# Kernel optimization log

Measured on AMD Instinct MI355X. Metric: run time of the kernel, lower is better.

The kernel has to match this reference:

```python
import jax, jax.numpy as jnp
import numpy as np

L, B, D = 2048, 16, 1024
SCALE_X = (1.0 + 2.0 * float(np.exp(0.0))) ** 0.5  # rescale=True, highway_bias=0 -> sqrt(3)


def setup_inputs() -> dict:
    key = jax.random.key(0)
    k1, k2, k3 = jax.random.split(key, 3)
    x = jax.random.normal(k1, (L, B, D), dtype=jnp.float32)
    c0 = jnp.zeros((B, D), dtype=jnp.float32)
    # Xavier-ish scale (3/d)^0.5 as in reset_parameters
    val_range = (3.0 / D) ** 0.5
    weight = jax.random.uniform(k2, (D, 3 * D), dtype=jnp.float32,
                                minval=-val_range, maxval=val_range)
    weight_c = jax.random.uniform(k3, (2 * D,), dtype=jnp.float32,
                                  minval=-val_range, maxval=val_range)
    bias = jnp.zeros((2 * D,), dtype=jnp.float32)
    return {"x": x, "c0": c0, "weight": weight, "weight_c": weight_c, "bias": bias}


def _sru_forward(x, c0, weight, weight_c, bias):
    # u = x @ W, viewed as [L, B, D, 3] (k = 3)
    u = jnp.einsum('lbi,io->lbo', x, weight).reshape(L, B, D, 3)
    fw, rw = weight_c[:D], weight_c[D:]      # per-feature recurrent gate weights
    fb, rb = bias[:D], bias[D:]              # forget / reset biases
    u0 = u[..., 0]                           # [L, B, D] candidate
    u1 = u[..., 1] + fb                      # forget pre-activation
    u2 = u[..., 2] + rb                      # reset pre-activation
    xp = x * SCALE_X                         # highway term (k==3, skip via x)

    def step(c_prev, inputs):
        u0_t, u1_t, u2_t, xp_t = inputs
        f = jax.nn.sigmoid(u1_t + c_prev * fw)
        r = jax.nn.sigmoid(u2_t + c_prev * rw)
        c = u0_t + (c_prev - u0_t) * f
        g = c  # activation_type == 0 (identity)
        h = xp_t + (g - xp_t) * r
        return c, h

    c_final, h = jax.lax.scan(step, c0, (u0, u1, u2, xp))
    return h, c_final


def reference(x, c0, weight, weight_c, bias):
    return _sru_forward(x, c0, weight, weight_c, bias)
```

## Files before the change

kernel.cpp:

```cpp
#include <hip/hip_runtime.h>
#include <stdint.h>

#define L_DIM 2048
#define B_DIM 16
#define D_DIM 1024
#define M_DIM 32768
#define K_DIM 1024
#define N_DIM 3072
#define SCALE_X 1.7320508075688772f

typedef __attribute__((ext_vector_type(8))) short short8;
typedef __attribute__((ext_vector_type(8))) unsigned short ushort8;
typedef __attribute__((ext_vector_type(4))) float f32x4;

__device__ __forceinline__ float bf2f(uint32_t b) {
    union { uint32_t u; float f; } v; v.u = b << 16; return v.f;
}
__device__ __forceinline__ uint16_t f2bf(float f) {
    union { float f; uint32_t u; } v; v.f = f;
    uint32_t u = v.u;
    return (uint16_t)((u + 0x7FFFu + ((u >> 16) & 1u)) >> 16);
}

__device__ __forceinline__ void gl16(const uint16_t* g, uint16_t* l) {
    __builtin_amdgcn_global_load_lds(
        (const __attribute__((address_space(1))) void*)g,
        (__attribute__((address_space(3))) void*)l,
        16 , 0, 0);
}

__device__ __forceinline__ void fence_all() {
    asm volatile("" ::: "memory");
    __builtin_amdgcn_sched_barrier(0);
}
__device__ __forceinline__ void barrier_hard() {
    fence_all();
    __builtin_amdgcn_s_barrier();
    fence_all();
}

__global__ void __launch_bounds__(256)
prep_w_kernel(const float* __restrict__ w, uint16_t* __restrict__ wt) {
    __shared__ uint16_t tile[32][33];
    int bid = blockIdx.x;
    int kt = (bid & 31) * 32;
    int nt = (bid >> 5) * 32;
    int tx = threadIdx.x & 31;
    int ty = threadIdx.x >> 5;
#pragma unroll
    for (int r = 0; r < 32; r += 8)
        tile[ty + r][tx] = f2bf(w[(size_t)(kt + ty + r) * N_DIM + nt + tx]);
    __syncthreads();
#pragma unroll
    for (int r = 0; r < 32; r += 8)
        wt[(size_t)(nt + ty + r) * K_DIM + kt + tx] = tile[tx][ty + r];
}

__global__ void __launch_bounds__(256)
prep_x_kernel(const float* __restrict__ x, uint16_t* __restrict__ xb) {
    size_t i = (size_t)blockIdx.x * 256 + threadIdx.x;
    const float4 a = *(const float4*)(x + i * 8);
    const float4 b = *(const float4*)(x + i * 8 + 4);
    ushort8 o;
    o[0] = f2bf(a.x); o[1] = f2bf(a.y); o[2] = f2bf(a.z); o[3] = f2bf(a.w);
    o[4] = f2bf(b.x); o[5] = f2bf(b.y); o[6] = f2bf(b.z); o[7] = f2bf(b.w);
    *(ushort8*)(xb + i * 8) = o;
}

__global__ void __launch_bounds__(512, 2)
gemm_8ph_kernel(const uint16_t* __restrict__ Ab,
                const uint16_t* __restrict__ Bt,
                uint16_t* __restrict__ u01,
                uint16_t* __restrict__ u2p)
{
    __shared__ uint16_t lds[65536];

    int bid = blockIdx.x;
    int mg = bid / 96;
    int tt = bid - mg * 96;
    int ntile = tt >> 3;
    int mtile = mg * 8 + (tt & 7);
    int m0 = mtile * 256;
    int n0 = ntile * 256;

    int t = threadIdx.x;
    int lane = t & 63;
    int w = t >> 6;
    int wm = (w >> 2) * 128;
    int wn = (w & 3) * 64;

    int row0 = t >> 3;
    int slot = t & 7;
    int swz_c = (slot ^ (row0 & 7)) * 8;
    const uint16_t* pA = Ab + (((size_t)(m0 + row0)) << 10) + swz_c;
    const uint16_t* pB = Bt + (((size_t)(n0 + row0)) << 10) + swz_c;

    int frow = lane & 15;
    int fkb = (lane >> 4) * 16;

    f32x4 acc[8][4] = {};
    short8 aF[4][2];
    short8 bF[4][2];

#define STAGE(hh, Tn) { \
    const uint16_t* gs = (((hh) < 2) ? pA : pB) + ((size_t)((hh) & 1) * 131072) + (size_t)(Tn) * 64; \
    uint16_t* ld = lds + nxtO + (hh) * 8192 + t * 8; \
    gl16(gs, ld); gl16(gs + 65536, ld + 4096); }

#define RD_A(mh) { \
    _Pragma("unroll") for (int mf = 0; mf < 4; mf++) \
    _Pragma("unroll") for (int ks = 0; ks < 2; ks++) { \
        int r = wm + (mh) * 64 + mf * 16 + frow; \
        int cb = (ks * 64 + fkb) ^ ((r & 7) << 4); \
        aF[mf][ks] = *(const short8*)(lds + curA + r * 64 + (cb >> 1)); } }

#define RD_B() { \
    _Pragma("unroll") for (int nf = 0; nf < 4; nf++) \
    _Pragma("unroll") for (int ks = 0; ks < 2; ks++) { \
        int r = wn + nf * 16 + frow; \
        int cb = (ks * 64 + fkb) ^ ((r & 7) << 4); \
        bF[nf][ks] = *(const short8*)(lds + curB + r * 64 + (cb >> 1)); } }

#define QM(mh, nh) { \
    __builtin_amdgcn_s_setprio(1); \
    _Pragma("unroll") for (int mf = 0; mf < 4; mf++) \
    _Pragma("unroll") for (int nj = 0; nj < 2; nj++) \
    _Pragma("unroll") for (int ks = 0; ks < 2; ks++) \
        acc[(mh) * 4 + mf][(nh) * 2 + nj] = __builtin_amdgcn_mfma_f32_16x16x32_bf16( \
            aF[mf][ks], bF[(nh) * 2 + nj][ks], acc[(mh) * 4 + mf][(nh) * 2 + nj], 0, 0, 0); \
    __builtin_amdgcn_s_setprio(0); }

    {
        int nxtO = 0;
        STAGE(0, 0); STAGE(1, 0); STAGE(2, 0); STAGE(3, 0);
    }

    for (int T = 0; T < 15; ++T) {
        int cur = T & 1;
        int curA = cur * 32768;
        int curB = curA + 16384;
        int nxtO = (cur ^ 1) * 32768;

        barrier_hard();
        STAGE(0, T + 1);
        fence_all();
        asm volatile("s_waitcnt vmcnt(2)" ::: "memory");
        barrier_hard();
        RD_B();
        RD_A(0);
        QM(0, 0);
        fence_all();
        STAGE(1, T + 1);
        fence_all();
        QM(0, 1);
        RD_A(1);
        fence_all();
        STAGE(2, T + 1);
        fence_all();
        QM(1, 1);
        fence_all();
        STAGE(3, T + 1);
        fence_all();
        QM(1, 0);
    }

    {
        int curA = 32768;
        int curB = curA + 16384;
        barrier_hard();
        asm volatile("s_waitcnt vmcnt(0)" ::: "memory");
        barrier_hard();
        RD_B();
        RD_A(0);
        QM(0, 0);
        QM(0, 1);
        RD_A(1);
        QM(1, 1);
        QM(1, 0);
    }

#undef STAGE
#undef RD_A
#undef RD_B
#undef QM

    int colf = lane & 15;
    int rowq = (lane >> 4) * 4;
#pragma unroll
    for (int i = 0; i < 8; i++) {
#pragma unroll
        for (int j = 0; j < 4; j++) {
            int gcol = n0 + wn + j * 16 + colf;
            int dq = gcol / 3;
            int cm = gcol - dq * 3;
#pragma unroll
            for (int r = 0; r < 4; r++) {
                int grow = m0 + wm + i * 16 + rowq + r;
                uint16_t v = f2bf(acc[i][j][r]);
                if (cm < 2) u01[(size_t)grow * 2048 + dq * 2 + cm] = v;
                else        u2p[(size_t)grow * 1024 + dq] = v;
            }
        }
    }
}

__global__ void __launch_bounds__(256)
gemm_kernel(const float* __restrict__ A32,
            const uint16_t* __restrict__ Bt,
            uint16_t* __restrict__ u01,
            uint16_t* __restrict__ u2p)
{
    __shared__ uint16_t As[128 * 32];
    __shared__ uint16_t Bs[128 * 32];

    int bid = blockIdx.x;
    int mg = bid / 192;
    int tt = bid - mg * 192;
    int ntile = tt >> 3;
    int mtile = mg * 8 + (tt & 7);
    int m0 = mtile * 128;
    int n0 = ntile * 128;

    int t = threadIdx.x;
    int lane = t & 63;
    int w = t >> 6;
    int wm = (w >> 1) * 64;
    int wn = (w & 1) * 64;

    f32x4 acc[4][4] = {};

    int frow = lane & 15;
    int fk = (lane >> 4) * 8;

    for (int kt = 0; kt < K_DIM; kt += 32) {
#pragma unroll
        for (int c = 0; c < 4; c++) {
            int idx = c * 256 + t;
            int row = idx >> 3;
            int ko = (idx & 7) * 4;
            float4 v = *(const float4*)(A32 + (size_t)(m0 + row) * K_DIM + kt + ko);
            ushort4 o;
            o.x = f2bf(v.x); o.y = f2bf(v.y); o.z = f2bf(v.z); o.w = f2bf(v.w);
            *(ushort4*)(As + row * 32 + ko) = o;
        }
#pragma unroll
        for (int c = 0; c < 2; c++) {
            int idx = c * 256 + t;
            int row = idx >> 2;
            int ko = (idx & 3) * 8;
            short8 v = *(const short8*)(Bt + (size_t)(n0 + row) * K_DIM + kt + ko);
            *(short8*)(Bs + row * 32 + ko) = v;
        }
        __syncthreads();

        short8 af[4], bfr[4];
#pragma unroll
        for (int i = 0; i < 4; i++) {
            af[i]  = *(const short8*)(As + (wm + i * 16 + frow) * 32 + fk);
            bfr[i] = *(const short8*)(Bs + (wn + i * 16 + frow) * 32 + fk);
        }
#pragma unroll
        for (int i = 0; i < 4; i++)
#pragma unroll
            for (int j = 0; j < 4; j++)
                acc[i][j] = __builtin_amdgcn_mfma_f32_16x16x32_bf16(af[i], bfr[j], acc[i][j], 0, 0, 0);
        __syncthreads();
    }

    int colf = lane & 15;
    int rowq = (lane >> 4) * 4;
#pragma unroll
    for (int i = 0; i < 4; i++) {
#pragma unroll
        for (int j = 0; j < 4; j++) {
            int gcol = n0 + wn + j * 16 + colf;
            int dq = gcol / 3;
            int cm = gcol - dq * 3;
#pragma unroll
            for (int r = 0; r < 4; r++) {
                int grow = m0 + wm + i * 16 + rowq + r;
                uint16_t v = f2bf(acc[i][j][r]);
                if (cm < 2) u01[(size_t)grow * 2048 + dq * 2 + cm] = v;
                else        u2p[(size_t)grow * 1024 + dq] = v;
            }
        }
    }
}

__global__ void __launch_bounds__(64)
scan_c_kernel(const uint32_t* u01,
              uint16_t* u2io,
              const float* __restrict__ c0,
              const float* __restrict__ wc,
              const float* __restrict__ bias,
              float* out)
{
    int cid = blockIdx.x * 64 + threadIdx.x;
    int d = cid & (D_DIM - 1);
    float fw = wc[d], rw = wc[D_DIM + d];
    float fb = bias[d], rb = bias[D_DIM + d];
    float c = c0[cid];

    constexpr int P = 16;
    const int STEP = B_DIM * D_DIM;
    uint32_t b01[P];
    uint16_t b2[P];
#pragma unroll
    for (int j = 0; j < P; j++) {
        b01[j] = u01[cid + j * STEP];
        b2[j]  = u2io[cid + j * STEP];
    }

    for (int lb = 0; lb < L_DIM; lb += P) {
#pragma unroll
        for (int j = 0; j < P; j++) {
            int l = lb + j;
            uint32_t v01 = b01[j];
            float u2 = bf2f((uint32_t)b2[j]);

            int ln = l + P; if (ln > L_DIM - 1) ln = L_DIM - 1;
            b01[j] = u01[cid + ln * STEP];
            b2[j]  = u2io[cid + ln * STEP];

            float u0 = bf2f(v01 & 0xFFFFu);
            float u1 = bf2f(v01 >> 16);
            float cp = c;
            float ef = __expf(-(u1 + fb + cp * fw));
            float f = __builtin_amdgcn_rcpf(1.0f + ef);
            c = u0 + (cp - u0) * f;
            float rarg = u2 + rb + cp * rw;
            out[l * STEP + cid] = c;
            u2io[l * STEP + cid] = f2bf(rarg);
        }
    }
    out[L_DIM * STEP + cid] = c;
}

__global__ void __launch_bounds__(256)
h_kernel(float* out,
         const uint16_t* __restrict__ rargp,
         const float* __restrict__ x)
{
    size_t i = ((size_t)blockIdx.x * 256 + threadIdx.x) * 4;

    f32x4 cv = *(const f32x4*)(out + i);
    f32x4 xv = *(const f32x4*)(x + i);
    ushort4 uv = *(const ushort4*)(rargp + i);

    float ra[4] = { bf2f(uv.x), bf2f(uv.y), bf2f(uv.z), bf2f(uv.w) };
    f32x4 h;
#pragma unroll
    for (int e = 0; e < 4; e++) {
        float xp = xv[e] * SCALE_X;
        float er = __expf(-ra[e]);
        float r = __builtin_amdgcn_rcpf(1.0f + er);
        h[e] = xp + (cv[e] - xp) * r;
    }
    *(f32x4*)(out + i) = h;
}

extern "C" void kernel_launch(void* const* d_in, const int* in_sizes, int n_in,
                              void* d_out, int out_size, void* d_ws, size_t ws_size,
                              hipStream_t stream) {
    const float* x    = (const float*)d_in[0];
    const float* c0   = (const float*)d_in[1];
    const float* w    = (const float*)d_in[2];
    const float* wc   = (const float*)d_in[3];
    const float* bias = (const float*)d_in[4];

    uint16_t* wt  = (uint16_t*)d_ws;
    uint16_t* u2p = (uint16_t*)((char*)d_ws + 6291456);
    const size_t XB_OFF = 6291456 + (size_t)M_DIM * D_DIM * 2;
    const size_t WS_NEED = XB_OFF + (size_t)M_DIM * K_DIM * 2;

    uint16_t* u01 = (uint16_t*)d_out;
    float* out = (float*)d_out;

    prep_w_kernel<<<(K_DIM / 32) * (N_DIM / 32), 256, 0, stream>>>(w, wt);

    if (ws_size >= WS_NEED) {
        uint16_t* xb = (uint16_t*)((char*)d_ws + XB_OFF);
        prep_x_kernel<<<(M_DIM * K_DIM / 8) / 256, 256, 0, stream>>>(x, xb);
        gemm_8ph_kernel<<<(M_DIM / 256) * (N_DIM / 256), 512, 0, stream>>>(xb, wt, u01, u2p);
    } else {
        gemm_kernel<<<(M_DIM / 128) * (N_DIM / 128), 256, 0, stream>>>(x, wt, u01, u2p);
    }

    scan_c_kernel<<<(B_DIM * D_DIM) / 64, 64, 0, stream>>>((const uint32_t*)u01, u2p,
                                                           c0, wc, bias, out);
    h_kernel<<<(M_DIM * D_DIM / 4) / 256, 256, 0, stream>>>(out, u2p, x);
}
```

Measured before the change: 699.4 us.

## Move reset-gate math out of the serial scan and pre-permute weight columns

The weight transpose now permutes output columns so the GEMM epilogue writes u0/u1 interleaved and u2 contiguously, with no per-element divide by 3. The scan no longer reads u2 or computes the reset argument. It only writes packed bf16 (c_prev, c) pairs, which cuts traffic in the latency-bound serial loop. The h kernel recomputes the reset gate from u2, c_prev, rw and rb, and processes 8 elements per thread. The trade-off is lower precision, since c is stored as bf16 before h is formed, and the scan writes into the same output buffer that h_kernel later overwrites.

```diff
diff --git a/kernel.cpp b/kernel.cpp
--- a/kernel.cpp
+++ b/kernel.cpp
@@ -12,6 +12,7 @@
 typedef __attribute__((ext_vector_type(8))) short short8;
 typedef __attribute__((ext_vector_type(8))) unsigned short ushort8;
 typedef __attribute__((ext_vector_type(4))) float f32x4;
+typedef __attribute__((ext_vector_type(4))) unsigned int u32x4;
 
 __device__ __forceinline__ float bf2f(uint32_t b) {
     union { uint32_t u; float f; } v; v.u = b << 16; return v.f;
@@ -37,6 +38,12 @@
     fence_all();
     __builtin_amdgcn_s_barrier();
     fence_all();
+}
+
+__device__ __forceinline__ int perm_n(int n) {
+    int dq = n / 3;
+    int cm = n - dq * 3;
+    return (cm < 2) ? (dq * 2 + cm) : (2048 + dq);
 }
 
 __global__ void __launch_bounds__(256)
@@ -52,8 +59,10 @@
         tile[ty + r][tx] = f2bf(w[(size_t)(kt + ty + r) * N_DIM + nt + tx]);
     __syncthreads();
 #pragma unroll
-    for (int r = 0; r < 32; r += 8)
-        wt[(size_t)(nt + ty + r) * K_DIM + kt + tx] = tile[tx][ty + r];
+    for (int r = 0; r < 32; r += 8) {
+        int s = perm_n(nt + ty + r);
+        wt[(size_t)s * K_DIM + kt + tx] = tile[tx][ty + r];
+    }
 }
 
 __global__ void __launch_bounds__(256)
@@ -191,14 +200,12 @@
 #pragma unroll
         for (int j = 0; j < 4; j++) {
             int gcol = n0 + wn + j * 16 + colf;
-            int dq = gcol / 3;
-            int cm = gcol - dq * 3;
 #pragma unroll
             for (int r = 0; r < 4; r++) {
                 int grow = m0 + wm + i * 16 + rowq + r;
                 uint16_t v = f2bf(acc[i][j][r]);
-                if (cm < 2) u01[(size_t)grow * 2048 + dq * 2 + cm] = v;
-                else        u2p[(size_t)grow * 1024 + dq] = v;
+                if (gcol < 2048) u01[(size_t)grow * 2048 + gcol] = v;
+                else             u2p[(size_t)grow * 1024 + (gcol - 2048)] = v;
             }
         }
     }
@@ -274,14 +281,12 @@
 #pragma unroll
         for (int j = 0; j < 4; j++) {
             int gcol = n0 + wn + j * 16 + colf;
-            int dq = gcol / 3;
-            int cm = gcol - dq * 3;
 #pragma unroll
             for (int r = 0; r < 4; r++) {
                 int grow = m0 + wm + i * 16 + rowq + r;
                 uint16_t v = f2bf(acc[i][j][r]);
-                if (cm < 2) u01[(size_t)grow * 2048 + dq * 2 + cm] = v;
-                else        u2p[(size_t)grow * 1024 + dq] = v;
+                if (gcol < 2048) u01[(size_t)grow * 2048 + gcol] = v;
+                else             u2p[(size_t)grow * 1024 + (gcol - 2048)] = v;
             }
         }
     }
@@ -289,7 +294,7 @@
 
 __global__ void __launch_bounds__(64)
 scan_c_kernel(const uint32_t* u01,
-              uint16_t* u2io,
+              uint32_t* cpack,
               const float* __restrict__ c0,
               const float* __restrict__ wc,
               const float* __restrict__ bias,
@@ -297,30 +302,24 @@
 {
     int cid = blockIdx.x * 64 + threadIdx.x;
     int d = cid & (D_DIM - 1);
-    float fw = wc[d], rw = wc[D_DIM + d];
-    float fb = bias[d], rb = bias[D_DIM + d];
+    float fw = wc[d];
+    float fb = bias[d];
     float c = c0[cid];
 
     constexpr int P = 16;
     const int STEP = B_DIM * D_DIM;
     uint32_t b01[P];
-    uint16_t b2[P];
-#pragma unroll
-    for (int j = 0; j < P; j++) {
-        b01[j] = u01[cid + j * STEP];
-        b2[j]  = u2io[cid + j * STEP];
-    }
+#pragma unroll
+    for (int j = 0; j < P; j++) b01[j] = u01[cid + j * STEP];
 
     for (int lb = 0; lb < L_DIM; lb += P) {
 #pragma unroll
         for (int j = 0; j < P; j++) {
             int l = lb + j;
             uint32_t v01 = b01[j];
-            float u2 = bf2f((uint32_t)b2[j]);
 
             int ln = l + P; if (ln > L_DIM - 1) ln = L_DIM - 1;
             b01[j] = u01[cid + ln * STEP];
-            b2[j]  = u2io[cid + ln * STEP];
 
             float u0 = bf2f(v01 & 0xFFFFu);
             float u1 = bf2f(v01 >> 16);
@@ -328,9 +327,7 @@
             float ef = __expf(-(u1 + fb + cp * fw));
             float f = __builtin_amdgcn_rcpf(1.0f + ef);
             c = u0 + (cp - u0) * f;
-            float rarg = u2 + rb + cp * rw;
-            out[l * STEP + cid] = c;
-            u2io[l * STEP + cid] = f2bf(rarg);
+            cpack[l * STEP + cid] = (uint32_t)f2bf(cp) | ((uint32_t)f2bf(c) << 16);
         }
     }
     out[L_DIM * STEP + cid] = c;
@@ -338,25 +335,49 @@
 
 __global__ void __launch_bounds__(256)
 h_kernel(float* out,
-         const uint16_t* __restrict__ rargp,
-         const float* __restrict__ x)
+         const uint16_t* __restrict__ u2p,
+         const float* __restrict__ x,
+         const float* __restrict__ wc,
+         const float* __restrict__ bias)
 {
-    size_t i = ((size_t)blockIdx.x * 256 + threadIdx.x) * 4;
-
-    f32x4 cv = *(const f32x4*)(out + i);
-    f32x4 xv = *(const f32x4*)(x + i);
-    ushort4 uv = *(const ushort4*)(rargp + i);
-
-    float ra[4] = { bf2f(uv.x), bf2f(uv.y), bf2f(uv.z), bf2f(uv.w) };
-    f32x4 h;
+    size_t i = ((size_t)blockIdx.x * 256 + threadIdx.x) * 8;
+    int d0 = (int)(i & (D_DIM - 1));
+
+    u32x4 cv0 = *(const u32x4*)((const uint32_t*)out + i);
+    u32x4 cv1 = *(const u32x4*)((const uint32_t*)out + i + 4);
+    f32x4 xv0 = *(const f32x4*)(x + i);
+    f32x4 xv1 = *(const f32x4*)(x + i + 4);
+    ushort8 uv = *(const ushort8*)(u2p + i);
+    f32x4 rw0 = *(const f32x4*)(wc + D_DIM + d0);
+    f32x4 rw1 = *(const f32x4*)(wc + D_DIM + d0 + 4);
+    f32x4 rb0 = *(const f32x4*)(bias + D_DIM + d0);
+    f32x4 rb1 = *(const f32x4*)(bias + D_DIM + d0 + 4);
+
+    f32x4 h0, h1;
 #pragma unroll
     for (int e = 0; e < 4; e++) {
-        float xp = xv[e] * SCALE_X;
-        float er = __expf(-ra[e]);
+        uint32_t v = cv0[e];
+        float cprev = bf2f(v & 0xFFFFu);
+        float cl = bf2f(v >> 16);
+        float u2 = bf2f((uint32_t)(unsigned short)uv[e]);
+        float xp = xv0[e] * SCALE_X;
+        float er = __expf(-(u2 + rb0[e] + cprev * rw0[e]));
         float r = __builtin_amdgcn_rcpf(1.0f + er);
-        h[e] = xp + (cv[e] - xp) * r;
-    }
-    *(f32x4*)(out + i) = h;
+        h0[e] = xp + (cl - xp) * r;
+    }
+#pragma unroll
+    for (int e = 0; e < 4; e++) {
+        uint32_t v = cv1[e];
+        float cprev = bf2f(v & 0xFFFFu);
+        float cl = bf2f(v >> 16);
+        float u2 = bf2f((uint32_t)(unsigned short)uv[e + 4]);
+        float xp = xv1[e] * SCALE_X;
+        float er = __expf(-(u2 + rb1[e] + cprev * rw1[e]));
+        float r = __builtin_amdgcn_rcpf(1.0f + er);
+        h1[e] = xp + (cl - xp) * r;
+    }
+    *(f32x4*)(out + i) = h0;
+    *(f32x4*)(out + i + 4) = h1;
 }
 
 extern "C" void kernel_launch(void* const* d_in, const int* in_sizes, int n_in,
@@ -386,7 +407,8 @@
         gemm_kernel<<<(M_DIM / 128) * (N_DIM / 128), 256, 0, stream>>>(x, wt, u01, u2p);
     }
 
-    scan_c_kernel<<<(B_DIM * D_DIM) / 64, 64, 0, stream>>>((const uint32_t*)u01, u2p,
+    scan_c_kernel<<<(B_DIM * D_DIM) / 64, 64, 0, stream>>>((const uint32_t*)u01,
+                                                           (uint32_t*)d_out,
                                                            c0, wc, bias, out);
-    h_kernel<<<(M_DIM * D_DIM / 4) / 256, 256, 0, stream>>>(out, u2p, x);
-}
+    h_kernel<<<(M_DIM * D_DIM / 8) / 256, 256, 0, stream>>>(out, u2p, x, wc, bias);
+}
```

Measured after the change: 642.0 us. -8.2%, faster.
